# Kernel tuning notes

Measured on AMD Instinct MI355X. Metric: run time of the kernel, lower is better.

## Reference

```python
import jax, jax.numpy as jnp
import numpy as np

B, D, H, W = 32, 64, 64, 64
K = 1024

def setup_inputs() -> dict:
    key = jax.random.key(0)
    k1, k2 = jax.random.split(key)
    x = jax.random.normal(k1, (B, D, H, W), dtype=jnp.float32)
    # nn.Parameter(torch.rand(embeddings_dim, num_embeddings)) -> uniform [0,1)
    emb = jax.random.uniform(k2, (D, K), dtype=jnp.float32)
    return {"x": x, "emb": emb}


def reference(x, emb):
    # x: [B, D, H, W], emb: [D, K]
    b, d, h, w = x.shape
    xf = jnp.transpose(x, (0, 2, 3, 1)).reshape(-1, d)  # [N, D], N = B*H*W
    # squared L2 distance (same argmin as torch.norm(.,2) distance)
    d2 = (
        jnp.sum(xf * xf, axis=-1, keepdims=True)
        - 2.0 * (xf @ emb)
        + jnp.sum(emb * emb, axis=0)
    )  # [N, K]
    argmin = jnp.argmin(d2, axis=-1)  # [N]
    # gather codebook vectors: emb.T[argmin] -> [N, D]
    q = jnp.take(emb.T, argmin, axis=0)
    result = jnp.transpose(q.reshape(b, h, w, d), (0, 3, 1, 2))  # [B, D, H, W]
    return result, argmin.reshape(b, h, w)
```

## Files before the change

### kernel.cpp

```cpp
#include <hip/hip_runtime.h>


using half8  = __attribute__((ext_vector_type(8))) _Float16;
using f32x16 = __attribute__((ext_vector_type(16))) float;
using u32x4  = __attribute__((ext_vector_type(4))) unsigned int;

static __device__ __forceinline__ unsigned int f16bits(_Float16 h) {
    union { _Float16 f; unsigned short u; } cv; cv.f = h; return (unsigned int)cv.u;
}

__global__ void prep_kernel(const float* __restrict__ emb,
                            unsigned int* __restrict__ e2p,
                            _Float16* __restrict__ eTh,
                            _Float16* __restrict__ eTl) {
    const int b = blockIdx.x;
    const int t = threadIdx.x;
    if (b < 32) {
        const int c = b >> 2;
        const int k = (b & 3) * 256 + t;
        half8 hv, lv;
#pragma unroll
        for (int j = 0; j < 8; ++j) {
            float v = emb[(c * 8 + j) * 1024 + k];
            _Float16 h = (_Float16)v;
            hv[j] = h;
            lv[j] = (_Float16)(v - (float)h);
        }
        *(half8*)(eTh + k * 64 + c * 8) = hv;
        *(half8*)(eTl + k * 64 + c * 8) = lv;
    } else {
        const int k = (b - 32) * 256 + t;
        float s = 0.f;
#pragma unroll
        for (int d = 0; d < 64; ++d) {
            float v = emb[(d << 10) + k];
            s = fmaf(v, v, s);
        }
        const float e2h = 0.5f * s;
        _Float16 h = (_Float16)e2h;
        _Float16 l = (_Float16)(e2h - (float)h);
        e2p[k] = f16bits(h) | (f16bits(l) << 16);
    }
}

__launch_bounds__(256, 4)
__global__ void vq_kernel(const float* __restrict__ x,
                          const _Float16* __restrict__ eTh,
                          const _Float16* __restrict__ eTl,
                          const unsigned int* __restrict__ e2p,
                          const float* __restrict__ emb,
                          float* __restrict__ outq,
                          float* __restrict__ outidx) {
    __shared__ __align__(16) _Float16 sB[2][4096];

    const int tx = threadIdx.x;
    const int n0 = blockIdx.x * 128;
    const int bb = n0 >> 12;
    const int hw = n0 & 4095;
    const float* xbase = x + bb * 262144 + hw;

    const int lane = tx & 63;
    const int w    = tx >> 6;
    const int c    = lane & 31;
    const int hi   = lane >> 5;
    const int pxb  = w << 5;

    half8 xh[4], xl[4];
#pragma unroll
    for (int ch = 0; ch < 4; ++ch) {
#pragma unroll
        for (int j = 0; j < 8; ++j) {
            float v = -xbase[(ch * 16 + hi * 8 + j) * 4096 + pxb + c];
            _Float16 h = (_Float16)v;
            xh[ch][j] = h;
            xl[ch][j] = (_Float16)(v - (float)h);
        }
    }
    asm volatile("" ::: "memory");

    half8 bones = {};
    if (hi == 0) { bones[0] = (_Float16)1.0f; bones[1] = (_Float16)1.0f; }

    int Dofs[4];
#pragma unroll
    for (int ch = 0; ch < 4; ++ch) {
        const int y = c * 128 + ch * 32 + hi * 16;
        Dofs[ch] = y ^ ((c & 7) << 4);
    }

    const int Lb = tx * 16;
    const int Sb = Lb ^ (((Lb >> 7) & 7) << 4);
    const char* gH = (const char*)eTh + Sb;
    const char* gL = (const char*)eTl + Sb;

#define STAGE(BUF, TT)                                                        \
    {                                                                         \
        __builtin_amdgcn_global_load_lds(                                     \
            (const __attribute__((address_space(1))) unsigned int*)(gH + ((TT) << 12)), \
            (__attribute__((address_space(3))) unsigned int*)(sB[BUF] + (w << 9)),       \
            16, 0, 0);                                                        \
        __builtin_amdgcn_global_load_lds(                                     \
            (const __attribute__((address_space(1))) unsigned int*)(gL + ((TT) << 12)), \
            (__attribute__((address_space(3))) unsigned int*)(sB[BUF] + 2048 + (w << 9)),\
            16, 0, 0);                                                        \
    }

    float brun[16];
#pragma unroll
    for (int i = 0; i < 16; ++i) brun[i] = 3.4e38f;
    float best = 3.4e38f;
    int   bt   = 0;

    STAGE(0, 0);
    __syncthreads();

#pragma unroll 1
    for (int t = 0; t < 32; ++t) {
        const int cur = t & 1;
        if (t < 31) STAGE(cur ^ 1, t + 1);

        const unsigned int ev = e2p[(t << 5) + c];
        union { u32x4 u; half8 h; } ae2u;
        ae2u.u = (u32x4){ (hi == 0) ? ev : 0u, 0u, 0u, 0u };
        const half8 ae2 = ae2u.h;

        const char* bbase = (const char*)sB[cur];
        half8 bh_[4], bl_[4];
#pragma unroll
        for (int ch = 0; ch < 4; ++ch) {
            bh_[ch] = *(const half8*)(bbase + Dofs[ch]);
            bl_[ch] = *(const half8*)(bbase + 4096 + Dofs[ch]);
        }

        f32x16 a = {};
        a = __builtin_amdgcn_mfma_f32_32x32x16_f16(ae2, bones, a, 0, 0, 0);
#pragma unroll
        for (int ch = 0; ch < 4; ++ch)
            a = __builtin_amdgcn_mfma_f32_32x32x16_f16(bl_[ch], xl[ch], a, 0, 0, 0);
#pragma unroll
        for (int ch = 0; ch < 4; ++ch)
            a = __builtin_amdgcn_mfma_f32_32x32x16_f16(bl_[ch], xh[ch], a, 0, 0, 0);
#pragma unroll
        for (int ch = 0; ch < 4; ++ch)
            a = __builtin_amdgcn_mfma_f32_32x32x16_f16(bh_[ch], xl[ch], a, 0, 0, 0);
#pragma unroll
        for (int ch = 0; ch < 4; ++ch)
            a = __builtin_amdgcn_mfma_f32_32x32x16_f16(bh_[ch], xh[ch], a, 0, 0, 0);

#pragma unroll
        for (int r = 0; r < 16; ++r) brun[r] = fminf(brun[r], a[r]);
        float m0 = fminf(fminf(a[0], a[1]),  fminf(a[2], a[3]));
        float m1 = fminf(fminf(a[4], a[5]),  fminf(a[6], a[7]));
        float m2 = fminf(fminf(a[8], a[9]),  fminf(a[10], a[11]));
        float m3 = fminf(fminf(a[12], a[13]), fminf(a[14], a[15]));
        float m  = fminf(fminf(m0, m1), fminf(m2, m3));
        if (m < best) bt = t;
        best = fminf(best, m);

        __syncthreads();
    }

    int rst = 0;
#pragma unroll
    for (int rr = 15; rr >= 0; --rr)
        if (brun[rr] == best) rst = rr;
    const int row = (rst & 3) + 8 * (rst >> 2) + 4 * hi;
    int bk = (bt << 5) + row;

    {
        float ov = __shfl_xor(best, 32, 64);
        int   ok = __shfl_xor(bk, 32, 64);
        if (ov < best || (ov == best && ok < bk)) { best = ov; bk = ok; }
    }

    int* samin = (int*)&sB[0][0];
    if (lane < 32) samin[pxb + c] = bk;
    __syncthreads();

    if (tx < 128) outidx[n0 + tx] = (float)samin[tx];

    const int p = tx & 127;
    const int drow = tx >> 7;
    const int amin = samin[p];
    float* obase = outq + bb * 262144 + hw + p;
#pragma unroll
    for (int it = 0; it < 32; ++it) {
        int d = (it << 1) + drow;
        obase[d * 4096] = emb[d * 1024 + amin];
    }
}

extern "C" void kernel_launch(void* const* d_in, const int* in_sizes, int n_in,
                              void* d_out, int out_size, void* d_ws, size_t ws_size,
                              hipStream_t stream) {
    const float* x   = (const float*)d_in[0];
    const float* emb = (const float*)d_in[1];
    float* outq   = (float*)d_out;
    float* outidx = outq + 8388608;

    unsigned int* e2p = (unsigned int*)d_ws;
    _Float16*     eTh = (_Float16*)((char*)d_ws + 4096);
    _Float16*     eTl = (_Float16*)((char*)d_ws + 4096 + 131072);

    prep_kernel<<<36, 256, 0, stream>>>(emb, e2p, eTh, eTl);
    vq_kernel<<<1024, 256, 0, stream>>>(x, eTh, eTl, e2p, emb, outq, outidx);
}
```

Before: 154.6 us.

## Prepack codebook in MFMA fragment layout and load directly to registers

The prep kernel now writes the fp16 hi/lo codebook already laid out in per-lane MFMA operand order. The main kernel drops the LDS double buffer and per-iteration barriers, and each wave loads its B fragments straight from global/L2 into registers, software-pipelined two tiles deep. The goal is to remove LDS staging, bank-swizzle reads and block-wide syncs. In exchange, every wave re-reads the codebook from cache, register pressure rises, and launch bounds drop to 3 blocks per SIMD.

New measurement: 161.5 us. 4.5% more time.

```diff
diff --git a/kernel.cpp b/kernel.cpp
--- a/kernel.cpp
+++ b/kernel.cpp
@@ -11,25 +11,31 @@
 
 __global__ void prep_kernel(const float* __restrict__ emb,
                             unsigned int* __restrict__ e2p,
-                            _Float16* __restrict__ eTh,
-                            _Float16* __restrict__ eTl) {
+                            _Float16* __restrict__ eTph,
+                            _Float16* __restrict__ eTpl) {
     const int b = blockIdx.x;
-    const int t = threadIdx.x;
+    const int tx = threadIdx.x;
     if (b < 32) {
-        const int c = b >> 2;
-        const int k = (b & 3) * 256 + t;
+        const int g  = b * 256 + tx;
+        const int t  = g >> 8;
+        const int ch = (g >> 6) & 3;
+        const int l  = g & 63;
+        const int c  = l & 31;
+        const int hi = l >> 5;
+        const int k  = t * 32 + c;
         half8 hv, lv;
 #pragma unroll
         for (int j = 0; j < 8; ++j) {
-            float v = emb[(c * 8 + j) * 1024 + k];
+            float v = emb[(ch * 16 + hi * 8 + j) * 1024 + k];
             _Float16 h = (_Float16)v;
             hv[j] = h;
             lv[j] = (_Float16)(v - (float)h);
         }
-        *(half8*)(eTh + k * 64 + c * 8) = hv;
-        *(half8*)(eTl + k * 64 + c * 8) = lv;
+        const int o = t * 2048 + ch * 512 + l * 8;
+        *(half8*)(eTph + o) = hv;
+        *(half8*)(eTpl + o) = lv;
     } else {
-        const int k = (b - 32) * 256 + t;
+        const int k = (b - 32) * 256 + tx;
         float s = 0.f;
 #pragma unroll
         for (int d = 0; d < 64; ++d) {
@@ -43,15 +49,15 @@
     }
 }
 
-__launch_bounds__(256, 4)
+__launch_bounds__(256, 3)
 __global__ void vq_kernel(const float* __restrict__ x,
-                          const _Float16* __restrict__ eTh,
-                          const _Float16* __restrict__ eTl,
+                          const _Float16* __restrict__ eTph,
+                          const _Float16* __restrict__ eTpl,
                           const unsigned int* __restrict__ e2p,
                           const float* __restrict__ emb,
                           float* __restrict__ outq,
                           float* __restrict__ outidx) {
-    __shared__ __align__(16) _Float16 sB[2][4096];
+    __shared__ int samin[128];
 
     const int tx = threadIdx.x;
     const int n0 = blockIdx.x * 128;
@@ -81,28 +87,59 @@
     half8 bones = {};
     if (hi == 0) { bones[0] = (_Float16)1.0f; bones[1] = (_Float16)1.0f; }
 
-    int Dofs[4];
-#pragma unroll
-    for (int ch = 0; ch < 4; ++ch) {
-        const int y = c * 128 + ch * 32 + hi * 16;
-        Dofs[ch] = y ^ ((c & 7) << 4);
-    }
-
-    const int Lb = tx * 16;
-    const int Sb = Lb ^ (((Lb >> 7) & 7) << 4);
-    const char* gH = (const char*)eTh + Sb;
-    const char* gL = (const char*)eTl + Sb;
-
-#define STAGE(BUF, TT)                                                        \
+    const char* pH = (const char*)eTph + (lane << 4);
+    const char* pL = (const char*)eTpl + (lane << 4);
+
+    half8 s0h0, s0h1, s0h2, s0h3, s0l0, s0l1, s0l2, s0l3;
+    half8 s1h0, s1h1, s1h2, s1h3, s1l0, s1l1, s1l2, s1l3;
+    unsigned int s0e, s1e;
+
+#define LOADF(S, TT)                                                          \
     {                                                                         \
-        __builtin_amdgcn_global_load_lds(                                     \
-            (const __attribute__((address_space(1))) unsigned int*)(gH + ((TT) << 12)), \
-            (__attribute__((address_space(3))) unsigned int*)(sB[BUF] + (w << 9)),       \
-            16, 0, 0);                                                        \
-        __builtin_amdgcn_global_load_lds(                                     \
-            (const __attribute__((address_space(1))) unsigned int*)(gL + ((TT) << 12)), \
-            (__attribute__((address_space(3))) unsigned int*)(sB[BUF] + 2048 + (w << 9)),\
-            16, 0, 0);                                                        \
+        const char* ph_ = pH + ((TT) << 12);                                  \
+        const char* pl_ = pL + ((TT) << 12);                                  \
+        S##h0 = *(const half8*)(ph_);                                         \
+        S##h1 = *(const half8*)(ph_ + 1024);                                  \
+        S##h2 = *(const half8*)(ph_ + 2048);                                  \
+        S##h3 = *(const half8*)(ph_ + 3072);                                  \
+        S##l0 = *(const half8*)(pl_);                                         \
+        S##l1 = *(const half8*)(pl_ + 1024);                                  \
+        S##l2 = *(const half8*)(pl_ + 2048);                                  \
+        S##l3 = *(const half8*)(pl_ + 3072);                                  \
+        S##e  = e2p[((TT) << 5) + c];                                         \
+    }
+
+#define COMPF(S, TT)                                                          \
+    {                                                                         \
+        union { u32x4 u; half8 h; } ae2u_;                                    \
+        ae2u_.u = (u32x4){ (hi == 0) ? S##e : 0u, 0u, 0u, 0u };               \
+        f32x16 a = {};                                                        \
+        a = __builtin_amdgcn_mfma_f32_32x32x16_f16(ae2u_.h, bones, a, 0, 0, 0); \
+        a = __builtin_amdgcn_mfma_f32_32x32x16_f16(S##l0, xl[0], a, 0, 0, 0); \
+        a = __builtin_amdgcn_mfma_f32_32x32x16_f16(S##l1, xl[1], a, 0, 0, 0); \
+        a = __builtin_amdgcn_mfma_f32_32x32x16_f16(S##l2, xl[2], a, 0, 0, 0); \
+        a = __builtin_amdgcn_mfma_f32_32x32x16_f16(S##l3, xl[3], a, 0, 0, 0); \
+        a = __builtin_amdgcn_mfma_f32_32x32x16_f16(S##l0, xh[0], a, 0, 0, 0); \
+        a = __builtin_amdgcn_mfma_f32_32x32x16_f16(S##l1, xh[1], a, 0, 0, 0); \
+        a = __builtin_amdgcn_mfma_f32_32x32x16_f16(S##l2, xh[2], a, 0, 0, 0); \
+        a = __builtin_amdgcn_mfma_f32_32x32x16_f16(S##l3, xh[3], a, 0, 0, 0); \
+        a = __builtin_amdgcn_mfma_f32_32x32x16_f16(S##h0, xl[0], a, 0, 0, 0); \
+        a = __builtin_amdgcn_mfma_f32_32x32x16_f16(S##h1, xl[1], a, 0, 0, 0); \
+        a = __builtin_amdgcn_mfma_f32_32x32x16_f16(S##h2, xl[2], a, 0, 0, 0); \
+        a = __builtin_amdgcn_mfma_f32_32x32x16_f16(S##h3, xl[3], a, 0, 0, 0); \
+        a = __builtin_amdgcn_mfma_f32_32x32x16_f16(S##h0, xh[0], a, 0, 0, 0); \
+        a = __builtin_amdgcn_mfma_f32_32x32x16_f16(S##h1, xh[1], a, 0, 0, 0); \
+        a = __builtin_amdgcn_mfma_f32_32x32x16_f16(S##h2, xh[2], a, 0, 0, 0); \
+        a = __builtin_amdgcn_mfma_f32_32x32x16_f16(S##h3, xh[3], a, 0, 0, 0); \
+        _Pragma("unroll")                                                     \
+        for (int r = 0; r < 16; ++r) brun[r] = fminf(brun[r], a[r]);          \
+        float m0 = fminf(fminf(a[0], a[1]),   fminf(a[2], a[3]));             \
+        float m1 = fminf(fminf(a[4], a[5]),   fminf(a[6], a[7]));             \
+        float m2 = fminf(fminf(a[8], a[9]),   fminf(a[10], a[11]));           \
+        float m3 = fminf(fminf(a[12], a[13]), fminf(a[14], a[15]));           \
+        float m  = fminf(fminf(m0, m1), fminf(m2, m3));                       \
+        if (m < best) bt = (TT);                                              \
+        best = fminf(best, m);                                                \
     }
 
     float brun[16];
@@ -111,54 +148,17 @@
     float best = 3.4e38f;
     int   bt   = 0;
 
-    STAGE(0, 0);
-    __syncthreads();
-
+    LOADF(s0, 0);
 #pragma unroll 1
-    for (int t = 0; t < 32; ++t) {
-        const int cur = t & 1;
-        if (t < 31) STAGE(cur ^ 1, t + 1);
-
-        const unsigned int ev = e2p[(t << 5) + c];
-        union { u32x4 u; half8 h; } ae2u;
-        ae2u.u = (u32x4){ (hi == 0) ? ev : 0u, 0u, 0u, 0u };
-        const half8 ae2 = ae2u.h;
-
-        const char* bbase = (const char*)sB[cur];
-        half8 bh_[4], bl_[4];
-#pragma unroll
-        for (int ch = 0; ch < 4; ++ch) {
-            bh_[ch] = *(const half8*)(bbase + Dofs[ch]);
-            bl_[ch] = *(const half8*)(bbase + 4096 + Dofs[ch]);
-        }
-
-        f32x16 a = {};
-        a = __builtin_amdgcn_mfma_f32_32x32x16_f16(ae2, bones, a, 0, 0, 0);
-#pragma unroll
-        for (int ch = 0; ch < 4; ++ch)
-            a = __builtin_amdgcn_mfma_f32_32x32x16_f16(bl_[ch], xl[ch], a, 0, 0, 0);
-#pragma unroll
-        for (int ch = 0; ch < 4; ++ch)
-            a = __builtin_amdgcn_mfma_f32_32x32x16_f16(bl_[ch], xh[ch], a, 0, 0, 0);
-#pragma unroll
-        for (int ch = 0; ch < 4; ++ch)
-            a = __builtin_amdgcn_mfma_f32_32x32x16_f16(bh_[ch], xl[ch], a, 0, 0, 0);
-#pragma unroll
-        for (int ch = 0; ch < 4; ++ch)
-            a = __builtin_amdgcn_mfma_f32_32x32x16_f16(bh_[ch], xh[ch], a, 0, 0, 0);
-
-#pragma unroll
-        for (int r = 0; r < 16; ++r) brun[r] = fminf(brun[r], a[r]);
-        float m0 = fminf(fminf(a[0], a[1]),  fminf(a[2], a[3]));
-        float m1 = fminf(fminf(a[4], a[5]),  fminf(a[6], a[7]));
-        float m2 = fminf(fminf(a[8], a[9]),  fminf(a[10], a[11]));
-        float m3 = fminf(fminf(a[12], a[13]), fminf(a[14], a[15]));
-        float m  = fminf(fminf(m0, m1), fminf(m2, m3));
-        if (m < best) bt = t;
-        best = fminf(best, m);
-
-        __syncthreads();
-    }
+    for (int t = 0; t < 30; t += 2) {
+        LOADF(s1, t + 1);
+        COMPF(s0, t)
+        LOADF(s0, t + 2);
+        COMPF(s1, t + 1)
+    }
+    LOADF(s1, 31);
+    COMPF(s0, 30)
+    COMPF(s1, 31)
 
     int rst = 0;
 #pragma unroll
@@ -173,7 +173,6 @@
         if (ov < best || (ov == best && ok < bk)) { best = ov; bk = ok; }
     }
 
-    int* samin = (int*)&sB[0][0];
     if (lane < 32) samin[pxb + c] = bk;
     __syncthreads();
 
@@ -198,10 +197,10 @@
     float* outq   = (float*)d_out;
     float* outidx = outq + 8388608;
 
-    unsigned int* e2p = (unsigned int*)d_ws;
-    _Float16*     eTh = (_Float16*)((char*)d_ws + 4096);
-    _Float16*     eTl = (_Float16*)((char*)d_ws + 4096 + 131072);
-
-    prep_kernel<<<36, 256, 0, stream>>>(emb, e2p, eTh, eTl);
-    vq_kernel<<<1024, 256, 0, stream>>>(x, eTh, eTl, e2p, emb, outq, outidx);
-}
+    unsigned int* e2p  = (unsigned int*)d_ws;
+    _Float16*     eTph = (_Float16*)((char*)d_ws + 4096);
+    _Float16*     eTpl = (_Float16*)((char*)d_ws + 4096 + 131072);
+
+    prep_kernel<<<36, 256, 0, stream>>>(emb, e2p, eTph, eTpl);
+    vq_kernel<<<1024, 256, 0, stream>>>(x, eTph, eTpl, e2p, emb, outq, outidx);
+}
```
